# Kernel tuning notes

Hardware: AMD Instinct MI355X
Metric: run time of the kernel (lower is better)

## Reference

```python
import jax, jax.numpy as jnp
import numpy as np

B, S, D, H = 2, 2048, 2048, 16
DH = D // H  # 128
ROPE_BASE = 10000.0


def setup_inputs() -> dict:
    key = jax.random.key(0)
    ks = jax.random.split(key, 5)
    scale = 0.02
    return {
        "x": jax.random.normal(ks[0], (B, S, D), dtype=jnp.float32),
        "wq": jax.random.normal(ks[1], (D, D), dtype=jnp.float32) * scale,
        "wk": jax.random.normal(ks[2], (D, D), dtype=jnp.float32) * scale,
        "wv": jax.random.normal(ks[3], (D, D), dtype=jnp.float32) * scale,
        "wo": jax.random.normal(ks[4], (D, D), dtype=jnp.float32) * scale,
    }


def _rope_cache(seq_len, dhead):
    # flash-attn RotaryEmbedding: inv_freq over even dims, full rotary_dim = dhead
    inv_freq = 1.0 / (ROPE_BASE ** (jnp.arange(0, dhead, 2, dtype=jnp.float32) / dhead))
    t = jnp.arange(seq_len, dtype=jnp.float32)
    freqs = jnp.einsum("s,d->sd", t, inv_freq)  # [S, DH/2]
    return jnp.cos(freqs), jnp.sin(freqs)


def _apply_rope_interleaved(t, cos, sin):
    # t: [B, S, H, DH]; interleaved pairs (t[...,0::2], t[...,1::2])
    te, to = t[..., 0::2], t[..., 1::2]
    c = cos[None, :, None, :]
    s = sin[None, :, None, :]
    re = te * c - to * s
    ro = te * s + to * c
    return jnp.stack([re, ro], axis=-1).reshape(t.shape)


def reference(x, wq, wk, wv, wo):
    b, s, d = x.shape
    q = (x @ wq).reshape(b, s, H, DH)
    k = (x @ wk).reshape(b, s, H, DH)
    v = (x @ wv).reshape(b, s, H, DH)

    cos, sin = _rope_cache(s, DH)
    q = _apply_rope_interleaved(q.astype(jnp.float32), cos, sin)
    k = _apply_rope_interleaved(k.astype(jnp.float32), cos, sin)

    # flash_attn_func(causal=True) semantics: bf16 inputs, fp32 softmax, scale 1/sqrt(dhead)
    qb = q.astype(jnp.bfloat16)
    kb = k.astype(jnp.bfloat16)
    vb = v.astype(jnp.bfloat16)
    scale = 1.0 / np.sqrt(DH)
    scores = jnp.einsum("bqhd,bkhd->bhqk", qb, kb,
                        preferred_element_type=jnp.float32) * scale
    causal = jnp.tril(jnp.ones((s, s), dtype=bool))
    scores = jnp.where(causal[None, None], scores, -jnp.inf)
    p = jax.nn.softmax(scores, axis=-1)  # fp32
    attn = jnp.einsum("bhqk,bkhd->bqhd", p.astype(jnp.bfloat16), vb,
                      preferred_element_type=jnp.float32)
    attn = attn.astype(jnp.bfloat16).astype(x.dtype)  # flash returns bf16, then .to(x)
    out = attn.reshape(b, s, d) @ wo
    return out
```

## Files before the change

### kernel.cpp

```cpp
#include <hip/hip_runtime.h>
#include <hip/hip_bf16.h>
#include <stdint.h>

#define B_SZ   2
#define S_LEN  2048
#define DMODEL 2048
#define NH     16
#define DHD    128

typedef __attribute__((ext_vector_type(8))) __bf16 bf16x8;
typedef __attribute__((ext_vector_type(4))) float  f32x4;
typedef __attribute__((ext_vector_type(4))) float  float4v;
typedef __attribute__((ext_vector_type(8))) unsigned short ushort8;
typedef __attribute__((ext_vector_type(4))) unsigned short ushort4v;

__device__ __forceinline__ unsigned short f2bf(float f) {
  unsigned int u = __float_as_uint(f);
  unsigned int r = (u + 0x7fffu + ((u >> 16) & 1u)) >> 16;
  return (unsigned short)r;
}

__device__ __forceinline__ unsigned int cvt_pk_bf16(float lo, float hi) {
  unsigned int r;
  asm("v_cvt_pk_bf16_f32 %0, %1, %2" : "=v"(r) : "v"(lo), "v"(hi));
  return r;
}

__device__ __forceinline__ void async_cp16(void* lds, const void* g) {
  __builtin_amdgcn_global_load_lds(
      (const __attribute__((address_space(1))) void*)g,
      (__attribute__((address_space(3))) void*)lds, 16, 0, 0);
}

__global__ __launch_bounds__(256) void k_cast_bf16(const float* __restrict__ in,
                                                   unsigned short* __restrict__ out,
                                                   int n4) {
  int i = blockIdx.x * 256 + threadIdx.x;
  if (i >= n4) return;
  float4v v = ((const float4v*)in)[i];
  ushort4v o;
  o[0] = f2bf(v[0]); o[1] = f2bf(v[1]); o[2] = f2bf(v[2]); o[3] = f2bf(v[3]);
  ((ushort4v*)out)[i] = o;
}

__global__ __launch_bounds__(256) void k_transpose_all(const float* __restrict__ w0,
                                                       const float* __restrict__ w1,
                                                       const float* __restrict__ w2,
                                                       const float* __restrict__ w3,
                                                       unsigned short* __restrict__ WTbase) {
  __shared__ unsigned short tile[64 * 72];
  const int z = blockIdx.z;
  const float* W = (z == 0) ? w0 : (z == 1) ? w1 : (z == 2) ? w2 : w3;
  unsigned short* WT = WTbase + (size_t)z * 4194304;
  const int n0 = blockIdx.x * 64;
  const int k0 = blockIdx.y * 64;
  const int t = threadIdx.x;
#pragma unroll
  for (int i = 0; i < 4; ++i) {
    int c = t + 256 * i;
    int r = c >> 4, c4 = c & 15;
    float4v v = *(const float4v*)(W + (size_t)(k0 + r) * DMODEL + n0 + c4 * 4);
    ushort4v o;
    o[0] = f2bf(v[0]); o[1] = f2bf(v[1]); o[2] = f2bf(v[2]); o[3] = f2bf(v[3]);
    *(ushort4v*)(&tile[r * 72 + c4 * 4]) = o;
  }
  __syncthreads();
#pragma unroll
  for (int i = 0; i < 2; ++i) {
    int c = t + 256 * i;
    int n = c >> 3, k8 = c & 7;
    ushort8 o;
#pragma unroll
    for (int j = 0; j < 8; ++j) o[j] = tile[(k8 * 8 + j) * 72 + n];
    *(ushort8*)(WT + (size_t)(n0 + n) * DMODEL + k0 + k8 * 8) = o;
  }
}

__global__ __launch_bounds__(256) void k_rope_table(float* __restrict__ cosT,
                                                    float* __restrict__ sinT) {
  int i = blockIdx.x * 256 + threadIdx.x;
  int s = i >> 6, dj = i & 63;
  float e = __expf(-9.210340371976184f * (float)dj * (1.0f / 64.0f));
  float f = (float)s * e;
  cosT[i] = cosf(f);
  sinT[i] = sinf(f);
}

template <int EPI>
__global__ __launch_bounds__(512, 2) void k_gemm128(
    const unsigned short* __restrict__ A,
    const unsigned short* __restrict__ BT,
    float* __restrict__ C0,
    unsigned short* __restrict__ Cq,
    unsigned short* __restrict__ Ck,
    unsigned short* __restrict__ Cv,
    const float* __restrict__ cosT,
    const float* __restrict__ sinT,
    int chn) {
  __shared__ char smem[98304];
  const int tid = threadIdx.x;

  const int xcd = blockIdx.x & 7;
  const int idx = blockIdx.x >> 3;
  const int bm = (xcd >> 2) * 16 + (idx & 15);
  const int bn = (xcd & 3) * chn + (idx >> 4);

  const int gs = (tid & 7) ^ ((tid >> 3) & 7);
  const unsigned short* Abase = A + (size_t)(bm * 128 + (tid >> 3)) * 2048 + gs * 8;
  const unsigned short* Bbase = BT + (size_t)(bn * 256 + (tid >> 3)) * 2048 + gs * 8;
  const int dstA = tid * 16;
  const int dstB = 16384 + tid * 16;

  const int lane = tid & 63, wid = tid >> 6;
  const int wr = wid >> 2, wcn = wid & 3;
  const int lr = lane & 15, hi = lane >> 4;
  int aoff[4][2], boff[4][2];
#pragma unroll
  for (int m = 0; m < 4; ++m) {
    int row = wr * 64 + m * 16 + lr;
#pragma unroll
    for (int k = 0; k < 2; ++k)
      aoff[m][k] = row * 128 + ((((k * 4 + hi)) ^ (row & 7)) << 4);
  }
#pragma unroll
  for (int n = 0; n < 4; ++n) {
    int row = wcn * 64 + n * 16 + lr;
#pragma unroll
    for (int k = 0; k < 2; ++k)
      boff[n][k] = 16384 + row * 128 + ((((k * 4 + hi)) ^ (row & 7)) << 4);
  }

  f32x4 acc[4][4];
#pragma unroll
  for (int m = 0; m < 4; ++m)
#pragma unroll
    for (int n = 0; n < 4; ++n) {
      f32x4 z = {0.f, 0.f, 0.f, 0.f};
      acc[m][n] = z;
    }

#define STG_A(c, t_) do {                                                   \
    const unsigned short* _s = Abase + (t_) * 64;                           \
    async_cp16(smem + (c) * 49152 + dstA, _s);                              \
    async_cp16(smem + (c) * 49152 + dstA + 8192, _s + 64 * 2048);           \
  } while (0)
#define STG_B(c, t_) do {                                                   \
    const unsigned short* _s = Bbase + (t_) * 64;                           \
    async_cp16(smem + (c) * 49152 + dstB, _s);                              \
    async_cp16(smem + (c) * 49152 + dstB + 8192, _s + 64 * 2048);           \
    async_cp16(smem + (c) * 49152 + dstB + 16384, _s + 128 * 2048);         \
    async_cp16(smem + (c) * 49152 + dstB + 24576, _s + 192 * 2048);         \
  } while (0)

  auto tile = [&](int T, int CC, bool DO_A, bool DO_B, int VM) __attribute__((always_inline)) {
    const char* Sb = smem + CC * 49152;
    bf16x8 a0[4], b0[4], a1[4], b1[4];
#pragma unroll
    for (int m = 0; m < 4; ++m) a0[m] = *(const bf16x8*)(Sb + aoff[m][0]);
#pragma unroll
    for (int n = 0; n < 4; ++n) b0[n] = *(const bf16x8*)(Sb + boff[n][0]);
    if (DO_A) STG_A(CC ^ 1, T + 1);
    asm volatile("s_waitcnt lgkmcnt(0)" ::: "memory");
    __builtin_amdgcn_sched_barrier(0);
    __builtin_amdgcn_s_setprio(1);
#pragma unroll
    for (int m = 0; m < 4; ++m) {
      acc[m][0] = __builtin_amdgcn_mfma_f32_16x16x32_bf16(a0[m], b0[0], acc[m][0], 0, 0, 0);
      acc[m][1] = __builtin_amdgcn_mfma_f32_16x16x32_bf16(a0[m], b0[1], acc[m][1], 0, 0, 0);
    }
    __builtin_amdgcn_s_setprio(0);
    __builtin_amdgcn_sched_barrier(0);
#pragma unroll
    for (int m = 0; m < 4; ++m) a1[m] = *(const bf16x8*)(Sb + aoff[m][1]);
#pragma unroll
    for (int n = 0; n < 4; ++n) b1[n] = *(const bf16x8*)(Sb + boff[n][1]);
    __builtin_amdgcn_sched_barrier(0);
    __builtin_amdgcn_s_setprio(1);
#pragma unroll
    for (int m = 0; m < 4; ++m) {
      acc[m][2] = __builtin_amdgcn_mfma_f32_16x16x32_bf16(a0[m], b0[2], acc[m][2], 0, 0, 0);
      acc[m][3] = __builtin_amdgcn_mfma_f32_16x16x32_bf16(a0[m], b0[3], acc[m][3], 0, 0, 0);
    }
    __builtin_amdgcn_s_setprio(0);
    __builtin_amdgcn_s_barrier();
    __builtin_amdgcn_sched_barrier(0);
    asm volatile("s_waitcnt lgkmcnt(0)" ::: "memory");
    __builtin_amdgcn_sched_barrier(0);
    if (DO_B) STG_B(CC, T + 2);
    __builtin_amdgcn_s_setprio(1);
#pragma unroll
    for (int m = 0; m < 4; ++m)
#pragma unroll
      for (int n = 0; n < 4; ++n)
        acc[m][n] = __builtin_amdgcn_mfma_f32_16x16x32_bf16(a1[m], b1[n], acc[m][n], 0, 0, 0);
    __builtin_amdgcn_s_setprio(0);
    if (VM == 0) asm volatile("s_waitcnt vmcnt(4)" ::: "memory");
    else if (VM == 1) asm volatile("s_waitcnt vmcnt(0)" ::: "memory");
    if (VM != 2) {
      __builtin_amdgcn_s_barrier();
      __builtin_amdgcn_sched_barrier(0);
    }
  };

  STG_B(0, 0);
  STG_A(0, 0);
  STG_B(1, 1);
  asm volatile("s_waitcnt vmcnt(4)" ::: "memory");
  __builtin_amdgcn_s_barrier();
  __builtin_amdgcn_sched_barrier(0);

  for (int it = 0; it < 15; ++it) {
    tile(2 * it, 0, true, true, 0);
    tile(2 * it + 1, 1, true, true, 0);
  }
  tile(30, 0, true, false, 1);
  tile(31, 1, false, false, 2);

  const int row_b = bm * 128 + wr * 64 + hi * 4;
  const int col_b = bn * 256 + wcn * 64 + lr;
  if (EPI == 0) {
#pragma unroll
    for (int m = 0; m < 4; ++m)
#pragma unroll
      for (int n = 0; n < 4; ++n) {
        int col = col_b + n * 16;
#pragma unroll
        for (int j = 0; j < 4; ++j) {
          int row = row_b + m * 16 + j;
          C0[(size_t)row * 2048 + col] = acc[m][n][j];
        }
      }
  } else {
    const int sel = bn >> 3;
#pragma unroll
    for (int m = 0; m < 4; ++m) {
#pragma unroll
      for (int n = 0; n < 4; ++n) {
        int col = col_b + n * 16;
        int hh = (col >> 7) & 15, d = col & 127;
        if (sel == 2) {
#pragma unroll
          for (int j = 0; j < 4; ++j) {
            int row = row_b + m * 16 + j;
            int b = row >> 11, s = row & 2047;
            Cv[((size_t)(b * NH + hh) * S_LEN + s) * DHD + d] = f2bf(acc[m][n][j]);
          }
        } else {
          unsigned short* dst = sel ? Ck : Cq;
          int dj = d >> 1;
          float sgn = (d & 1) ? 1.f : -1.f;
#pragma unroll
          for (int j = 0; j < 4; ++j) {
            int row = row_b + m * 16 + j;
            int b = row >> 11, s = row & 2047;
            float v = acc[m][n][j];
            float pp = __shfl_xor(v, 1);
            float cc = cosT[(s << 6) + dj];
            float sn = sinT[(s << 6) + dj];
            dst[((size_t)(b * NH + hh) * S_LEN + s) * DHD + d] = f2bf(v * cc + sgn * pp * sn);
          }
        }
      }
    }
  }
#undef STG_A
#undef STG_B
}

__global__ __launch_bounds__(256) void k_flash_attn(const unsigned short* __restrict__ Qg,
                                                    const unsigned short* __restrict__ Kg,
                                                    const unsigned short* __restrict__ Vg,
                                                    unsigned short* __restrict__ Og) {
  __shared__ unsigned short K_lds[2][64 * 128];
  __shared__ unsigned short VT_lds[2][128 * 64];

  const int pq = blockIdx.x, h = blockIdx.y, b = blockIdx.z;
  const int t = threadIdx.x;
  const int lane = t & 63, wave = t >> 6;
  const int hi = lane >> 4, lr = lane & 15;

  const size_t head = (size_t)(b * NH + h) * (size_t)(S_LEN * DHD);
  const unsigned short* Q = Qg + head;
  const unsigned short* Kp = Kg + head;
  const unsigned short* Vp = Vg + head;

  const int kr0 = t >> 4;
  const int kgc = (t & 15) ^ (kr0 & 7);
  const unsigned short* Kbase = Kp + (size_t)kr0 * DHD + kgc * 8;
  const int kdst = t * 16;

  const int vdc = t & 15, vsp0 = t >> 4;
  const unsigned short* Vbase = Vp + (size_t)(2 * vsp0) * DHD + vdc * 8;
  const int bo0 = 16 * ((vsp0 >> 1) & 3) + 8 * ((vsp0 >> 3) & 1) + 4 * (vsp0 & 1);

  const float sc = 0.08838834764831845f;

  for (int pass = 0; pass < 2; ++pass) {
    const int qt = (pass == 0) ? pq : (15 - pq);
    const int nt = 2 * (qt + 1);
    const int qb0 = qt * 128 + wave * 16;
    const int qb1 = qb0 + 64;

    bf16x8 qf0[4], qf1[4];
    {
      const unsigned short* qr0 = Q + (size_t)(qb0 + lr) * DHD;
      const unsigned short* qr1 = Q + (size_t)(qb1 + lr) * DHD;
#pragma unroll
      for (int kc = 0; kc < 4; ++kc) {
        qf0[kc] = *(const bf16x8*)(qr0 + kc * 32 + hi * 8);
        qf1[kc] = *(const bf16x8*)(qr1 + kc * 32 + hi * 8);
      }
    }

    f32x4 of0[8], of1[8];
#pragma unroll
    for (int i = 0; i < 8; ++i) {
      f32x4 z = {0.f, 0.f, 0.f, 0.f};
      of0[i] = z;
      of1[i] = z;
    }
    float mS0 = -INFINITY, mS1 = -INFINITY;
    float ls0 = 0.f, ls1 = 0.f;

    {
#pragma unroll
      for (int i = 0; i < 4; ++i)
        async_cp16((char*)K_lds[0] + kdst + i * 4096, Kbase + (size_t)(16 * i) * DHD);
      ushort8 va0 = *(const ushort8*)(Vbase);
      ushort8 vb0 = *(const ushort8*)(Vbase + DHD);
      ushort8 va1 = *(const ushort8*)(Vbase + (size_t)32 * DHD);
      ushort8 vb1 = *(const ushort8*)(Vbase + (size_t)33 * DHD);
#pragma unroll
      for (int j = 0; j < 8; ++j) {
        int row = vdc * 8 + j;
        int swz = ((j ^ vdc) & 7) << 4;
        *(unsigned int*)((char*)VT_lds[0] + row * 128 + (bo0 ^ swz)) =
            (unsigned int)va0[j] | ((unsigned int)vb0[j] << 16);
        *(unsigned int*)((char*)VT_lds[0] + row * 128 + ((bo0 | 64) ^ swz)) =
            (unsigned int)va1[j] | ((unsigned int)vb1[j] << 16);
      }
    }
    __syncthreads();

    for (int tt = 0; tt < nt; ++tt) {
      const int cur = tt & 1;
      const int kv0 = tt * 64;
      const bool more = (tt + 1 < nt);

      ushort8 va0, vb0, va1, vb1;
      if (more) {
        const unsigned short* ks = Kbase + (size_t)(kv0 + 64) * DHD;
#pragma unroll
        for (int i = 0; i < 4; ++i)
          async_cp16((char*)K_lds[cur ^ 1] + kdst + i * 4096, ks + (size_t)(16 * i) * DHD);
        const unsigned short* vs = Vbase + (size_t)(kv0 + 64) * DHD;
        va0 = *(const ushort8*)(vs);
        vb0 = *(const ushort8*)(vs + DHD);
        va1 = *(const ushort8*)(vs + (size_t)32 * DHD);
        vb1 = *(const ushort8*)(vs + (size_t)33 * DHD);
      }

      const char* Kb = (const char*)K_lds[cur];
      f32x4 sf0[4], sf1[4];
#pragma unroll
      for (int n = 0; n < 4; ++n) {
        f32x4 z = {0.f, 0.f, 0.f, 0.f};
        sf0[n] = z;
        sf1[n] = z;
      }
      __builtin_amdgcn_s_setprio(1);
#pragma unroll
      for (int n = 0; n < 4; ++n) {
        const int kr = n * 16 + lr;
        const int kswz = (kr & 7) << 4;
#pragma unroll
        for (int kc = 0; kc < 4; ++kc) {
          bf16x8 kf = *(const bf16x8*)(Kb + kr * 256 + ((kc * 64 + hi * 16) ^ kswz));
          sf0[n] = __builtin_amdgcn_mfma_f32_16x16x32_bf16(kf, qf0[kc], sf0[n], 0, 0, 0);
          sf1[n] = __builtin_amdgcn_mfma_f32_16x16x32_bf16(kf, qf1[kc], sf1[n], 0, 0, 0);
        }
      }
      __builtin_amdgcn_s_setprio(0);

      unsigned int pk0[4][2], pk1[4][2];
      float cb0[4], cb1[4];
      const bool act0 = kv0 <= qb0 + 15;
      const bool act1 = kv0 <= qb1 + 15;

#define SOFTMAX_SET(SF, MS, LS, PK, CB, QB, ACT) do {                        \
    if (ACT) {                                                               \
      float p_[4][4];                                                        \
      float mx = -INFINITY;                                                  \
      const int qrow_ = (QB) + lr;                                           \
      if (kv0 + 63 > (QB)) {                                                 \
        _Pragma("unroll")                                                    \
        for (int n = 0; n < 4; ++n)                                          \
          _Pragma("unroll")                                                  \
          for (int j = 0; j < 4; ++j) {                                      \
            int kvcol = kv0 + n * 16 + hi * 4 + j;                           \
            float v = (kvcol > qrow_) ? -INFINITY : SF[n][j];                \
            p_[n][j] = v;                                                    \
            mx = fmaxf(mx, v);                                               \
          }                                                                  \
      } else {                                                               \
        _Pragma("unroll")                                                    \
        for (int n = 0; n < 4; ++n)                                          \
          _Pragma("unroll")                                                  \
          for (int j = 0; j < 4; ++j) {                                      \
            float v = SF[n][j];                                              \
            p_[n][j] = v;                                                    \
            mx = fmaxf(mx, v);                                               \
          }                                                                  \
      }                                                                      \
      mx = fmaxf(mx, __shfl_xor(mx, 16));                                    \
      mx = fmaxf(mx, __shfl_xor(mx, 32));                                    \
      float mn = fmaxf(MS, mx);                                              \
      float corr = __expf((MS - mn) * sc);                                   \
      MS = mn;                                                               \
      float mns = mn * sc;                                                   \
      float rs = 0.f;                                                        \
      _Pragma("unroll")                                                      \
      for (int n = 0; n < 4; ++n)                                            \
        _Pragma("unroll")                                                    \
        for (int j = 0; j < 4; ++j) {                                        \
          float e = __expf(__builtin_fmaf(p_[n][j], sc, -mns));              \
          p_[n][j] = e;                                                      \
          rs += e;                                                           \
        }                                                                    \
      rs += __shfl_xor(rs, 16);                                              \
      rs += __shfl_xor(rs, 32);                                              \
      LS = LS * corr + rs;                                                   \
      _Pragma("unroll")                                                      \
      for (int n = 0; n < 4; ++n) {                                          \
        PK[n][0] = cvt_pk_bf16(p_[n][0], p_[n][1]);                          \
        PK[n][1] = cvt_pk_bf16(p_[n][2], p_[n][3]);                          \
      }                                                                      \
      _Pragma("unroll")                                                      \
      for (int j = 0; j < 4; ++j) CB[j] = __shfl(corr, hi * 4 + j);          \
    } else {                                                                 \
      _Pragma("unroll")                                                      \
      for (int n = 0; n < 4; ++n) { PK[n][0] = 0u; PK[n][1] = 0u; }          \
      _Pragma("unroll")                                                      \
      for (int j = 0; j < 4; ++j) CB[j] = 1.f;                               \
    }                                                                        \
  } while (0)

      SOFTMAX_SET(sf0, mS0, ls0, pk0, cb0, qb0, act0);
      SOFTMAX_SET(sf1, mS1, ls1, pk1, cb1, qb1, act1);
#undef SOFTMAX_SET

#pragma unroll
      for (int nd = 0; nd < 8; ++nd)
#pragma unroll
        for (int j = 0; j < 4; ++j) {
          of0[nd][j] *= cb0[j];
          of1[nd][j] *= cb1[j];
        }

      const char* Vb = (const char*)VT_lds[cur];
      __builtin_amdgcn_s_setprio(1);
#pragma unroll
      for (int kc = 0; kc < 2; ++kc) {
        union { unsigned int u[4]; bf16x8 v; } pa0, pa1;
        pa0.u[0] = pk0[2 * kc][0];     pa0.u[1] = pk0[2 * kc][1];
        pa0.u[2] = pk0[2 * kc + 1][0]; pa0.u[3] = pk0[2 * kc + 1][1];
        pa1.u[0] = pk1[2 * kc][0];     pa1.u[1] = pk1[2 * kc][1];
        pa1.u[2] = pk1[2 * kc + 1][0]; pa1.u[3] = pk1[2 * kc + 1][1];
#pragma unroll
        for (int nd = 0; nd < 8; ++nd) {
          const int vr = nd * 16 + lr;
          const int vswz = ((vr & 7) ^ ((vr >> 3) & 7)) << 4;
          bf16x8 vf = *(const bf16x8*)(Vb + vr * 128 + ((kc * 64 + hi * 16) ^ vswz));
          of0[nd] = __builtin_amdgcn_mfma_f32_16x16x32_bf16(pa0.v, vf, of0[nd], 0, 0, 0);
          of1[nd] = __builtin_amdgcn_mfma_f32_16x16x32_bf16(pa1.v, vf, of1[nd], 0, 0, 0);
        }
      }
      __builtin_amdgcn_s_setprio(0);

      if (more) {
        char* Vw = (char*)VT_lds[cur ^ 1];
#pragma unroll
        for (int j = 0; j < 8; ++j) {
          int row = vdc * 8 + j;
          int swz = ((j ^ vdc) & 7) << 4;
          *(unsigned int*)(Vw + row * 128 + (bo0 ^ swz)) =
              (unsigned int)va0[j] | ((unsigned int)vb0[j] << 16);
          *(unsigned int*)(Vw + row * 128 + ((bo0 | 64) ^ swz)) =
              (unsigned int)va1[j] | ((unsigned int)vb1[j] << 16);
        }
      }
      __syncthreads();
    }

    float inv0[4], inv1[4];
#pragma unroll
    for (int j = 0; j < 4; ++j) {
      inv0[j] = 1.0f / __shfl(ls0, hi * 4 + j);
      inv1[j] = 1.0f / __shfl(ls1, hi * 4 + j);
    }
#pragma unroll
    for (int nd = 0; nd < 8; ++nd)
#pragma unroll
      for (int j = 0; j < 4; ++j) {
        int qr0 = qb0 + hi * 4 + j;
        int qr1 = qb1 + hi * 4 + j;
        Og[((size_t)(b * S_LEN + qr0) * NH + h) * DHD + nd * 16 + lr] = f2bf(of0[nd][j] * inv0[j]);
        Og[((size_t)(b * S_LEN + qr1) * NH + h) * DHD + nd * 16 + lr] = f2bf(of1[nd][j] * inv1[j]);
      }
  }
}

extern "C" void kernel_launch(void* const* d_in, const int* in_sizes, int n_in,
                              void* d_out, int out_size, void* d_ws, size_t ws_size,
                              hipStream_t stream) {
  const float* x  = (const float*)d_in[0];
  const float* wq = (const float*)d_in[1];
  const float* wk = (const float*)d_in[2];
  const float* wv = (const float*)d_in[3];
  const float* wo = (const float*)d_in[4];
  float* out = (float*)d_out;

  char* ws = (char*)d_ws;
  unsigned short* xb    = (unsigned short*)(ws);
  unsigned short* wqT   = (unsigned short*)(ws + 16777216);
  unsigned short* woT   = (unsigned short*)(ws + 41943040);
  unsigned short* qb    = (unsigned short*)(ws + 50331648);
  unsigned short* kb    = (unsigned short*)(ws + 67108864);
  unsigned short* vb    = (unsigned short*)(ws + 83886080);
  float*          cosT  = (float*)(ws + 100663296);
  float*          sinT  = (float*)(ws + 101187584);
  unsigned short* attnb = xb;

  k_cast_bf16<<<8192, 256, 0, stream>>>(x, xb, 2097152);
  dim3 tg(32, 32, 4);
  k_transpose_all<<<tg, 256, 0, stream>>>(wq, wk, wv, wo, wqT);
  k_rope_table<<<512, 256, 0, stream>>>(cosT, sinT);

  k_gemm128<1><<<768, 512, 0, stream>>>(xb, wqT, nullptr, qb, kb, vb, cosT, sinT, 6);

  dim3 ga(8, 16, 2);
  k_flash_attn<<<ga, 256, 0, stream>>>(qb, kb, vb, attnb);

  k_gemm128<0><<<256, 512, 0, stream>>>(attnb, woT, out, nullptr, nullptr, nullptr,
                                        nullptr, nullptr, 2);
}
```

Baseline: 258.1 us.

## Use 256x256 QKV GEMM tiles, flatten flash-attn grid, hoist LDS fragment loads

```diff
diff --git a/kernel.cpp b/kernel.cpp
--- a/kernel.cpp
+++ b/kernel.cpp
@@ -86,16 +86,161 @@
   sinT[i] = sinf(f);
 }
 
-template <int EPI>
+__global__ __launch_bounds__(512, 2) void k_gemm256(
+    const unsigned short* __restrict__ A,
+    const unsigned short* __restrict__ BT,
+    unsigned short* __restrict__ Cq,
+    unsigned short* __restrict__ Ck,
+    unsigned short* __restrict__ Cv,
+    const float* __restrict__ cosT,
+    const float* __restrict__ sinT) {
+  __shared__ char smem[131072];
+  const int tid = threadIdx.x;
+
+  const int xcd = blockIdx.x & 7;
+  const int idx = blockIdx.x >> 3;
+  const int bm = (xcd >> 1) * 4 + (idx & 3);
+  const int bn = (xcd & 1) * 12 + (idx >> 2);
+
+  const int gs = (tid & 7) ^ ((tid >> 3) & 7);
+  const unsigned short* Abase = A + (size_t)(bm * 256 + (tid >> 3)) * 2048 + gs * 8;
+  const unsigned short* Bbase = BT + (size_t)(bn * 256 + (tid >> 3)) * 2048 + gs * 8;
+  const int dstA = tid * 16;
+  const int dstB = 32768 + tid * 16;
+
+  const int lane = tid & 63, wid = tid >> 6;
+  const int wr = wid >> 2, wcn = wid & 3;
+  const int lr = lane & 15, hi = lane >> 4;
+  const int sw0 = ((hi) ^ (lr & 7)) << 4;
+  const int sw1 = ((4 + hi) ^ (lr & 7)) << 4;
+  const int aB0 = (wr * 128 + lr) * 128 + sw0;
+  const int aB1 = (wr * 128 + lr) * 128 + sw1;
+  const int bB0 = 32768 + (wcn * 64 + lr) * 128 + sw0;
+  const int bB1 = 32768 + (wcn * 64 + lr) * 128 + sw1;
+
+  f32x4 acc[8][4];
+#pragma unroll
+  for (int m = 0; m < 8; ++m)
+#pragma unroll
+    for (int n = 0; n < 4; ++n) {
+      f32x4 z = {0.f, 0.f, 0.f, 0.f};
+      acc[m][n] = z;
+    }
+
+#define STG_A6(c, t_) do {                                                  \
+    const unsigned short* _s = Abase + (t_) * 64;                           \
+    async_cp16(smem + (c) * 65536 + dstA, _s);                              \
+    async_cp16(smem + (c) * 65536 + dstA + 8192, _s + (size_t)64 * 2048);   \
+    async_cp16(smem + (c) * 65536 + dstA + 16384, _s + (size_t)128 * 2048); \
+    async_cp16(smem + (c) * 65536 + dstA + 24576, _s + (size_t)192 * 2048); \
+  } while (0)
+#define STG_B6(c, t_) do {                                                  \
+    const unsigned short* _s = Bbase + (t_) * 64;                           \
+    async_cp16(smem + (c) * 65536 + dstB, _s);                              \
+    async_cp16(smem + (c) * 65536 + dstB + 8192, _s + (size_t)64 * 2048);   \
+    async_cp16(smem + (c) * 65536 + dstB + 16384, _s + (size_t)128 * 2048); \
+    async_cp16(smem + (c) * 65536 + dstB + 24576, _s + (size_t)192 * 2048); \
+  } while (0)
+
+  auto tile = [&](int T, int CC, bool DO_A, bool DO_B, int VM) __attribute__((always_inline)) {
+    const char* Sb = smem + CC * 65536;
+    bf16x8 a0[8], b0[4], b1[4];
+#pragma unroll
+    for (int n = 0; n < 4; ++n) b0[n] = *(const bf16x8*)(Sb + bB0 + n * 2048);
+#pragma unroll
+    for (int m = 0; m < 8; ++m) a0[m] = *(const bf16x8*)(Sb + aB0 + m * 2048);
+#pragma unroll
+    for (int n = 0; n < 4; ++n) b1[n] = *(const bf16x8*)(Sb + bB1 + n * 2048);
+    if (DO_A) STG_A6(CC ^ 1, T + 1);
+    asm volatile("s_waitcnt lgkmcnt(4)" ::: "memory");
+    __builtin_amdgcn_sched_barrier(0);
+    __builtin_amdgcn_s_setprio(1);
+#pragma unroll
+    for (int m = 0; m < 8; ++m)
+#pragma unroll
+      for (int n = 0; n < 4; ++n)
+        acc[m][n] = __builtin_amdgcn_mfma_f32_16x16x32_bf16(a0[m], b0[n], acc[m][n], 0, 0, 0);
+    __builtin_amdgcn_s_setprio(0);
+    __builtin_amdgcn_s_barrier();
+    __builtin_amdgcn_sched_barrier(0);
+    asm volatile("s_waitcnt lgkmcnt(0)" ::: "memory");
+    __builtin_amdgcn_sched_barrier(0);
+    if (DO_B) STG_B6(CC, T + 2);
+    bf16x8 a1[8];
+#pragma unroll
+    for (int m = 0; m < 8; ++m) a1[m] = *(const bf16x8*)(Sb + aB1 + m * 2048);
+    asm volatile("s_waitcnt lgkmcnt(0)" ::: "memory");
+    __builtin_amdgcn_sched_barrier(0);
+    __builtin_amdgcn_s_setprio(1);
+#pragma unroll
+    for (int m = 0; m < 8; ++m)
+#pragma unroll
+      for (int n = 0; n < 4; ++n)
+        acc[m][n] = __builtin_amdgcn_mfma_f32_16x16x32_bf16(a1[m], b1[n], acc[m][n], 0, 0, 0);
+    __builtin_amdgcn_s_setprio(0);
+    if (VM == 0) asm volatile("s_waitcnt vmcnt(4)" ::: "memory");
+    else if (VM == 1) asm volatile("s_waitcnt vmcnt(0)" ::: "memory");
+    if (VM != 2) {
+      __builtin_amdgcn_s_barrier();
+      __builtin_amdgcn_sched_barrier(0);
+    }
+  };
+
+  STG_B6(0, 0);
+  STG_A6(0, 0);
+  STG_B6(1, 1);
+  asm volatile("s_waitcnt vmcnt(4)" ::: "memory");
+  __builtin_amdgcn_s_barrier();
+  __builtin_amdgcn_sched_barrier(0);
+
+  for (int it = 0; it < 15; ++it) {
+    tile(2 * it, 0, true, true, 0);
+    tile(2 * it + 1, 1, true, true, 0);
+  }
+  tile(30, 0, true, false, 1);
+  tile(31, 1, false, false, 2);
+
+  const int row_b = bm * 256 + wr * 128 + hi * 4;
+  const int col_b = bn * 256 + wcn * 64 + lr;
+  const int sel = bn >> 3;
+#pragma unroll
+  for (int m = 0; m < 8; ++m) {
+#pragma unroll
+    for (int n = 0; n < 4; ++n) {
+      int col = col_b + n * 16;
+      int hh = (col >> 7) & 15, d = col & 127;
+      if (sel == 2) {
+#pragma unroll
+        for (int j = 0; j < 4; ++j) {
+          int row = row_b + m * 16 + j;
+          int b = row >> 11, s = row & 2047;
+          Cv[((size_t)(b * NH + hh) * S_LEN + s) * DHD + d] = f2bf(acc[m][n][j]);
+        }
+      } else {
+        unsigned short* dst = sel ? Ck : Cq;
+        int dj = d >> 1;
+        float sgn = (d & 1) ? 1.f : -1.f;
+#pragma unroll
+        for (int j = 0; j < 4; ++j) {
+          int row = row_b + m * 16 + j;
+          int b = row >> 11, s = row & 2047;
+          float v = acc[m][n][j];
+          float pp = __shfl_xor(v, 1);
+          float cc = cosT[(s << 6) + dj];
+          float sn = sinT[(s << 6) + dj];
+          dst[((size_t)(b * NH + hh) * S_LEN + s) * DHD + d] = f2bf(v * cc + sgn * pp * sn);
+        }
+      }
+    }
+  }
+#undef STG_A6
+#undef STG_B6
+}
+
 __global__ __launch_bounds__(512, 2) void k_gemm128(
     const unsigned short* __restrict__ A,
     const unsigned short* __restrict__ BT,
     float* __restrict__ C0,
-    unsigned short* __restrict__ Cq,
-    unsigned short* __restrict__ Ck,
-    unsigned short* __restrict__ Cv,
-    const float* __restrict__ cosT,
-    const float* __restrict__ sinT,
     int chn) {
   __shared__ char smem[98304];
   const int tid = threadIdx.x;
@@ -159,28 +304,20 @@
     for (int m = 0; m < 4; ++m) a0[m] = *(const bf16x8*)(Sb + aoff[m][0]);
 #pragma unroll
     for (int n = 0; n < 4; ++n) b0[n] = *(const bf16x8*)(Sb + boff[n][0]);
+    __builtin_amdgcn_sched_barrier(0);
+#pragma unroll
+    for (int m = 0; m < 4; ++m) a1[m] = *(const bf16x8*)(Sb + aoff[m][1]);
+#pragma unroll
+    for (int n = 0; n < 4; ++n) b1[n] = *(const bf16x8*)(Sb + boff[n][1]);
     if (DO_A) STG_A(CC ^ 1, T + 1);
-    asm volatile("s_waitcnt lgkmcnt(0)" ::: "memory");
+    asm volatile("s_waitcnt lgkmcnt(8)" ::: "memory");
     __builtin_amdgcn_sched_barrier(0);
     __builtin_amdgcn_s_setprio(1);
 #pragma unroll
-    for (int m = 0; m < 4; ++m) {
-      acc[m][0] = __builtin_amdgcn_mfma_f32_16x16x32_bf16(a0[m], b0[0], acc[m][0], 0, 0, 0);
-      acc[m][1] = __builtin_amdgcn_mfma_f32_16x16x32_bf16(a0[m], b0[1], acc[m][1], 0, 0, 0);
-    }
-    __builtin_amdgcn_s_setprio(0);
-    __builtin_amdgcn_sched_barrier(0);
-#pragma unroll
-    for (int m = 0; m < 4; ++m) a1[m] = *(const bf16x8*)(Sb + aoff[m][1]);
-#pragma unroll
-    for (int n = 0; n < 4; ++n) b1[n] = *(const bf16x8*)(Sb + boff[n][1]);
-    __builtin_amdgcn_sched_barrier(0);
-    __builtin_amdgcn_s_setprio(1);
-#pragma unroll
-    for (int m = 0; m < 4; ++m) {
-      acc[m][2] = __builtin_amdgcn_mfma_f32_16x16x32_bf16(a0[m], b0[2], acc[m][2], 0, 0, 0);
-      acc[m][3] = __builtin_amdgcn_mfma_f32_16x16x32_bf16(a0[m], b0[3], acc[m][3], 0, 0, 0);
-    }
+    for (int m = 0; m < 4; ++m)
+#pragma unroll
+      for (int n = 0; n < 4; ++n)
+        acc[m][n] = __builtin_amdgcn_mfma_f32_16x16x32_bf16(a0[m], b0[n], acc[m][n], 0, 0, 0);
     __builtin_amdgcn_s_setprio(0);
     __builtin_amdgcn_s_barrier();
     __builtin_amdgcn_sched_barrier(0);
@@ -218,51 +355,17 @@
 
   const int row_b = bm * 128 + wr * 64 + hi * 4;
   const int col_b = bn * 256 + wcn * 64 + lr;
-  if (EPI == 0) {
-#pragma unroll
-    for (int m = 0; m < 4; ++m)
-#pragma unroll
-      for (int n = 0; n < 4; ++n) {
-        int col = col_b + n * 16;
-#pragma unroll
-        for (int j = 0; j < 4; ++j) {
-          int row = row_b + m * 16 + j;
-          C0[(size_t)row * 2048 + col] = acc[m][n][j];
-        }
+#pragma unroll
+  for (int m = 0; m < 4; ++m)
+#pragma unroll
+    for (int n = 0; n < 4; ++n) {
+      int col = col_b + n * 16;
+#pragma unroll
+      for (int j = 0; j < 4; ++j) {
+        int row = row_b + m * 16 + j;
+        C0[(size_t)row * 2048 + col] = acc[m][n][j];
       }
-  } else {
-    const int sel = bn >> 3;
-#pragma unroll
-    for (int m = 0; m < 4; ++m) {
-#pragma unroll
-      for (int n = 0; n < 4; ++n) {
-        int col = col_b + n * 16;
-        int hh = (col >> 7) & 15, d = col & 127;
-        if (sel == 2) {
-#pragma unroll
-          for (int j = 0; j < 4; ++j) {
-            int row = row_b + m * 16 + j;
-            int b = row >> 11, s = row & 2047;
-            Cv[((size_t)(b * NH + hh) * S_LEN + s) * DHD + d] = f2bf(acc[m][n][j]);
-          }
-        } else {
-          unsigned short* dst = sel ? Ck : Cq;
-          int dj = d >> 1;
-          float sgn = (d & 1) ? 1.f : -1.f;
-#pragma unroll
-          for (int j = 0; j < 4; ++j) {
-            int row = row_b + m * 16 + j;
-            int b = row >> 11, s = row & 2047;
-            float v = acc[m][n][j];
-            float pp = __shfl_xor(v, 1);
-            float cc = cosT[(s << 6) + dj];
-            float sn = sinT[(s << 6) + dj];
-            dst[((size_t)(b * NH + hh) * S_LEN + s) * DHD + d] = f2bf(v * cc + sgn * pp * sn);
-          }
-        }
-      }
-    }
-  }
+    }
 #undef STG_A
 #undef STG_B
 }
@@ -274,7 +377,14 @@
   __shared__ unsigned short K_lds[2][64 * 128];
   __shared__ unsigned short VT_lds[2][128 * 64];
 
-  const int pq = blockIdx.x, h = blockIdx.y, b = blockIdx.z;
+  const int bx = blockIdx.x;
+  const int half = bx >> 8;
+  const int j5 = bx & 255;
+  const int ti = j5 >> 5;
+  const int hb = j5 & 31;
+  const int h = hb & 15, b = hb >> 4;
+  const int qt = half ? ti : (15 - ti);
+
   const int t = threadIdx.x;
   const int lane = t & 63, wave = t >> 6;
   const int hi = lane >> 4, lr = lane & 15;
@@ -295,97 +405,95 @@
 
   const float sc = 0.08838834764831845f;
 
-  for (int pass = 0; pass < 2; ++pass) {
-    const int qt = (pass == 0) ? pq : (15 - pq);
-    const int nt = 2 * (qt + 1);
-    const int qb0 = qt * 128 + wave * 16;
-    const int qb1 = qb0 + 64;
-
-    bf16x8 qf0[4], qf1[4];
-    {
-      const unsigned short* qr0 = Q + (size_t)(qb0 + lr) * DHD;
-      const unsigned short* qr1 = Q + (size_t)(qb1 + lr) * DHD;
+  const int nt = 2 * (qt + 1);
+  const int qb0 = qt * 128 + wave * 16;
+  const int qb1 = qb0 + 64;
+
+  bf16x8 qf0[4], qf1[4];
+  {
+    const unsigned short* qr0 = Q + (size_t)(qb0 + lr) * DHD;
+    const unsigned short* qr1 = Q + (size_t)(qb1 + lr) * DHD;
+#pragma unroll
+    for (int kc = 0; kc < 4; ++kc) {
+      qf0[kc] = *(const bf16x8*)(qr0 + kc * 32 + hi * 8);
+      qf1[kc] = *(const bf16x8*)(qr1 + kc * 32 + hi * 8);
+    }
+  }
+
+  f32x4 of0[8], of1[8];
+#pragma unroll
+  for (int i = 0; i < 8; ++i) {
+    f32x4 z = {0.f, 0.f, 0.f, 0.f};
+    of0[i] = z;
+    of1[i] = z;
+  }
+  float mS0 = -INFINITY, mS1 = -INFINITY;
+  float ls0 = 0.f, ls1 = 0.f;
+
+  {
+#pragma unroll
+    for (int i = 0; i < 4; ++i)
+      async_cp16((char*)K_lds[0] + kdst + i * 4096, Kbase + (size_t)(16 * i) * DHD);
+    ushort8 va0 = *(const ushort8*)(Vbase);
+    ushort8 vb0 = *(const ushort8*)(Vbase + DHD);
+    ushort8 va1 = *(const ushort8*)(Vbase + (size_t)32 * DHD);
+    ushort8 vb1 = *(const ushort8*)(Vbase + (size_t)33 * DHD);
+#pragma unroll
+    for (int j = 0; j < 8; ++j) {
+      int row = vdc * 8 + j;
+      int swz = ((j ^ vdc) & 7) << 4;
+      *(unsigned int*)((char*)VT_lds[0] + row * 128 + (bo0 ^ swz)) =
+          (unsigned int)va0[j] | ((unsigned int)vb0[j] << 16);
+      *(unsigned int*)((char*)VT_lds[0] + row * 128 + ((bo0 | 64) ^ swz)) =
+          (unsigned int)va1[j] | ((unsigned int)vb1[j] << 16);
+    }
+  }
+  __syncthreads();
+
+  for (int tt = 0; tt < nt; ++tt) {
+    const int cur = tt & 1;
+    const int kv0 = tt * 64;
+    const bool more = (tt + 1 < nt);
+
+    ushort8 va0, vb0, va1, vb1;
+    if (more) {
+      const unsigned short* ks = Kbase + (size_t)(kv0 + 64) * DHD;
+#pragma unroll
+      for (int i = 0; i < 4; ++i)
+        async_cp16((char*)K_lds[cur ^ 1] + kdst + i * 4096, ks + (size_t)(16 * i) * DHD);
+      const unsigned short* vs = Vbase + (size_t)(kv0 + 64) * DHD;
+      va0 = *(const ushort8*)(vs);
+      vb0 = *(const ushort8*)(vs + DHD);
+      va1 = *(const ushort8*)(vs + (size_t)32 * DHD);
+      vb1 = *(const ushort8*)(vs + (size_t)33 * DHD);
+    }
+
+    const char* Kb = (const char*)K_lds[cur];
+    f32x4 sf0[4], sf1[4];
+#pragma unroll
+    for (int n = 0; n < 4; ++n) {
+      f32x4 z = {0.f, 0.f, 0.f, 0.f};
+      sf0[n] = z;
+      sf1[n] = z;
+    }
+    __builtin_amdgcn_s_setprio(1);
+#pragma unroll
+    for (int n = 0; n < 4; ++n) {
+      const int kr = n * 16 + lr;
+      const int kswz = (kr & 7) << 4;
 #pragma unroll
       for (int kc = 0; kc < 4; ++kc) {
-        qf0[kc] = *(const bf16x8*)(qr0 + kc * 32 + hi * 8);
-        qf1[kc] = *(const bf16x8*)(qr1 + kc * 32 + hi * 8);
+        bf16x8 kf = *(const bf16x8*)(Kb + kr * 256 + ((kc * 64 + hi * 16) ^ kswz));
+        sf0[n] = __builtin_amdgcn_mfma_f32_16x16x32_bf16(kf, qf0[kc], sf0[n], 0, 0, 0);
+        sf1[n] = __builtin_amdgcn_mfma_f32_16x16x32_bf16(kf, qf1[kc], sf1[n], 0, 0, 0);
       }
     }
-
-    f32x4 of0[8], of1[8];
-#pragma unroll
-    for (int i = 0; i < 8; ++i) {
-      f32x4 z = {0.f, 0.f, 0.f, 0.f};
-      of0[i] = z;
-      of1[i] = z;
-    }
-    float mS0 = -INFINITY, mS1 = -INFINITY;
-    float ls0 = 0.f, ls1 = 0.f;
-
-    {
-#pragma unroll
-      for (int i = 0; i < 4; ++i)
-        async_cp16((char*)K_lds[0] + kdst + i * 4096, Kbase + (size_t)(16 * i) * DHD);
-      ushort8 va0 = *(const ushort8*)(Vbase);
-      ushort8 vb0 = *(const ushort8*)(Vbase + DHD);
-      ushort8 va1 = *(const ushort8*)(Vbase + (size_t)32 * DHD);
-      ushort8 vb1 = *(const ushort8*)(Vbase + (size_t)33 * DHD);
-#pragma unroll
-      for (int j = 0; j < 8; ++j) {
-        int row = vdc * 8 + j;
-        int swz = ((j ^ vdc) & 7) << 4;
-        *(unsigned int*)((char*)VT_lds[0] + row * 128 + (bo0 ^ swz)) =
-            (unsigned int)va0[j] | ((unsigned int)vb0[j] << 16);
-        *(unsigned int*)((char*)VT_lds[0] + row * 128 + ((bo0 | 64) ^ swz)) =
-            (unsigned int)va1[j] | ((unsigned int)vb1[j] << 16);
-      }
-    }
-    __syncthreads();
-
-    for (int tt = 0; tt < nt; ++tt) {
-      const int cur = tt & 1;
-      const int kv0 = tt * 64;
-      const bool more = (tt + 1 < nt);
-
-      ushort8 va0, vb0, va1, vb1;
-      if (more) {
-        const unsigned short* ks = Kbase + (size_t)(kv0 + 64) * DHD;
-#pragma unroll
-        for (int i = 0; i < 4; ++i)
-          async_cp16((char*)K_lds[cur ^ 1] + kdst + i * 4096, ks + (size_t)(16 * i) * DHD);
-        const unsigned short* vs = Vbase + (size_t)(kv0 + 64) * DHD;
-        va0 = *(const ushort8*)(vs);
-        vb0 = *(const ushort8*)(vs + DHD);
-        va1 = *(const ushort8*)(vs + (size_t)32 * DHD);
-        vb1 = *(const ushort8*)(vs + (size_t)33 * DHD);
-      }
-
-      const char* Kb = (const char*)K_lds[cur];
-      f32x4 sf0[4], sf1[4];
-#pragma unroll
-      for (int n = 0; n < 4; ++n) {
-        f32x4 z = {0.f, 0.f, 0.f, 0.f};
-        sf0[n] = z;
-        sf1[n] = z;
-      }
-      __builtin_amdgcn_s_setprio(1);
-#pragma unroll
-      for (int n = 0; n < 4; ++n) {
-        const int kr = n * 16 + lr;
-        const int kswz = (kr & 7) << 4;
-#pragma unroll
-        for (int kc = 0; kc < 4; ++kc) {
-          bf16x8 kf = *(const bf16x8*)(Kb + kr * 256 + ((kc * 64 + hi * 16) ^ kswz));
-          sf0[n] = __builtin_amdgcn_mfma_f32_16x16x32_bf16(kf, qf0[kc], sf0[n], 0, 0, 0);
-          sf1[n] = __builtin_amdgcn_mfma_f32_16x16x32_bf16(kf, qf1[kc], sf1[n], 0, 0, 0);
-        }
-      }
-      __builtin_amdgcn_s_setprio(0);
-
-      unsigned int pk0[4][2], pk1[4][2];
-      float cb0[4], cb1[4];
-      const bool act0 = kv0 <= qb0 + 15;
-      const bool act1 = kv0 <= qb1 + 15;
+    __builtin_amdgcn_s_setprio(0);
+
+    unsigned int pk0[4][2], pk1[4][2];
+    float cb0[4], cb1[4];
+    const bool act0 = kv0 <= qb0 + 15;
+    const bool act1 = kv0 <= qb1 + 15;
 
 #define SOFTMAX_SET(SF, MS, LS, PK, CB, QB, ACT) do {                        \
     if (ACT) {                                                               \
@@ -445,69 +553,68 @@
     }                                                                        \
   } while (0)
 
-      SOFTMAX_SET(sf0, mS0, ls0, pk0, cb0, qb0, act0);
-      SOFTMAX_SET(sf1, mS1, ls1, pk1, cb1, qb1, act1);
+    SOFTMAX_SET(sf0, mS0, ls0, pk0, cb0, qb0, act0);
+    SOFTMAX_SET(sf1, mS1, ls1, pk1, cb1, qb1, act1);
 #undef SOFTMAX_SET
 
 #pragma unroll
-      for (int nd = 0; nd < 8; ++nd)
-#pragma unroll
-        for (int j = 0; j < 4; ++j) {
-          of0[nd][j] *= cb0[j];
-          of1[nd][j] *= cb1[j];
-        }
-
-      const char* Vb = (const char*)VT_lds[cur];
-      __builtin_amdgcn_s_setprio(1);
-#pragma unroll
-      for (int kc = 0; kc < 2; ++kc) {
-        union { unsigned int u[4]; bf16x8 v; } pa0, pa1;
-        pa0.u[0] = pk0[2 * kc][0];     pa0.u[1] = pk0[2 * kc][1];
-        pa0.u[2] = pk0[2 * kc + 1][0]; pa0.u[3] = pk0[2 * kc + 1][1];
-        pa1.u[0] = pk1[2 * kc][0];     pa1.u[1] = pk1[2 * kc][1];
-        pa1.u[2] = pk1[2 * kc + 1][0]; pa1.u[3] = pk1[2 * kc + 1][1];
-#pragma unroll
-        for (int nd = 0; nd < 8; ++nd) {
-          const int vr = nd * 16 + lr;
-          const int vswz = ((vr & 7) ^ ((vr >> 3) & 7)) << 4;
-          bf16x8 vf = *(const bf16x8*)(Vb + vr * 128 + ((kc * 64 + hi * 16) ^ vswz));
-          of0[nd] = __builtin_amdgcn_mfma_f32_16x16x32_bf16(pa0.v, vf, of0[nd], 0, 0, 0);
-          of1[nd] = __builtin_amdgcn_mfma_f32_16x16x32_bf16(pa1.v, vf, of1[nd], 0, 0, 0);
-        }
+    for (int nd = 0; nd < 8; ++nd)
+#pragma unroll
+      for (int j = 0; j < 4; ++j) {
+        of0[nd][j] *= cb0[j];
+        of1[nd][j] *= cb1[j];
       }
-      __builtin_amdgcn_s_setprio(0);
-
-      if (more) {
-        char* Vw = (char*)VT_lds[cur ^ 1];
-#pragma unroll
-        for (int j = 0; j < 8; ++j) {
-          int row = vdc * 8 + j;
-          int swz = ((j ^ vdc) & 7) << 4;
-          *(unsigned int*)(Vw + row * 128 + (bo0 ^ swz)) =
-              (unsigned int)va0[j] | ((unsigned int)vb0[j] << 16);
-          *(unsigned int*)(Vw + row * 128 + ((bo0 | 64) ^ swz)) =
-              (unsigned int)va1[j] | ((unsigned int)vb1[j] << 16);
-        }
+
+    const char* Vb = (const char*)VT_lds[cur];
+    __builtin_amdgcn_s_setprio(1);
+#pragma unroll
+    for (int kc = 0; kc < 2; ++kc) {
+      union { unsigned int u[4]; bf16x8 v; } pa0, pa1;
+      pa0.u[0] = pk0[2 * kc][0];     pa0.u[1] = pk0[2 * kc][1];
+      pa0.u[2] = pk0[2 * kc + 1][0]; pa0.u[3] = pk0[2 * kc + 1][1];
+      pa1.u[0] = pk1[2 * kc][0];     pa1.u[1] = pk1[2 * kc][1];
+      pa1.u[2] = pk1[2 * kc + 1][0]; pa1.u[3] = pk1[2 * kc + 1][1];
+#pragma unroll
+      for (int nd = 0; nd < 8; ++nd) {
+        const int vr = nd * 16 + lr;
+        const int vswz = ((vr & 7) ^ ((vr >> 3) & 7)) << 4;
+        bf16x8 vf = *(const bf16x8*)(Vb + vr * 128 + ((kc * 64 + hi * 16) ^ vswz));
+        of0[nd] = __builtin_amdgcn_mfma_f32_16x16x32_bf16(pa0.v, vf, of0[nd], 0, 0, 0);
+        of1[nd] = __builtin_amdgcn_mfma_f32_16x16x32_bf16(pa1.v, vf, of1[nd], 0, 0, 0);
       }
-      __syncthreads();
-    }
-
-    float inv0[4], inv1[4];
+    }
+    __builtin_amdgcn_s_setprio(0);
+
+    if (more) {
+      char* Vw = (char*)VT_lds[cur ^ 1];
+#pragma unroll
+      for (int j = 0; j < 8; ++j) {
+        int row = vdc * 8 + j;
+        int swz = ((j ^ vdc) & 7) << 4;
+        *(unsigned int*)(Vw + row * 128 + (bo0 ^ swz)) =
+            (unsigned int)va0[j] | ((unsigned int)vb0[j] << 16);
+        *(unsigned int*)(Vw + row * 128 + ((bo0 | 64) ^ swz)) =
+            (unsigned int)va1[j] | ((unsigned int)vb1[j] << 16);
+      }
+    }
+    __syncthreads();
+  }
+
+  float inv0[4], inv1[4];
+#pragma unroll
+  for (int j = 0; j < 4; ++j) {
+    inv0[j] = 1.0f / __shfl(ls0, hi * 4 + j);
+    inv1[j] = 1.0f / __shfl(ls1, hi * 4 + j);
+  }
+#pragma unroll
+  for (int nd = 0; nd < 8; ++nd)
 #pragma unroll
     for (int j = 0; j < 4; ++j) {
-      inv0[j] = 1.0f / __shfl(ls0, hi * 4 + j);
-      inv1[j] = 1.0f / __shfl(ls1, hi * 4 + j);
-    }
-#pragma unroll
-    for (int nd = 0; nd < 8; ++nd)
-#pragma unroll
-      for (int j = 0; j < 4; ++j) {
-        int qr0 = qb0 + hi * 4 + j;
-        int qr1 = qb1 + hi * 4 + j;
-        Og[((size_t)(b * S_LEN + qr0) * NH + h) * DHD + nd * 16 + lr] = f2bf(of0[nd][j] * inv0[j]);
-        Og[((size_t)(b * S_LEN + qr1) * NH + h) * DHD + nd * 16 + lr] = f2bf(of1[nd][j] * inv1[j]);
-      }
-  }
+      int qr0 = qb0 + hi * 4 + j;
+      int qr1 = qb1 + hi * 4 + j;
+      Og[((size_t)(b * S_LEN + qr0) * NH + h) * DHD + nd * 16 + lr] = f2bf(of0[nd][j] * inv0[j]);
+      Og[((size_t)(b * S_LEN + qr1) * NH + h) * DHD + nd * 16 + lr] = f2bf(of1[nd][j] * inv1[j]);
+    }
 }
 
 extern "C" void kernel_launch(void* const* d_in, const int* in_sizes, int n_in,
@@ -536,11 +643,9 @@
   k_transpose_all<<<tg, 256, 0, stream>>>(wq, wk, wv, wo, wqT);
   k_rope_table<<<512, 256, 0, stream>>>(cosT, sinT);
 
-  k_gemm128<1><<<768, 512, 0, stream>>>(xb, wqT, nullptr, qb, kb, vb, cosT, sinT, 6);
-
-  dim3 ga(8, 16, 2);
-  k_flash_attn<<<ga, 256, 0, stream>>>(qb, kb, vb, attnb);
-
-  k_gemm128<0><<<256, 512, 0, stream>>>(attnb, woT, out, nullptr, nullptr, nullptr,
-                                        nullptr, nullptr, 2);
-}
+  k_gemm256<<<384, 512, 0, stream>>>(xb, wqT, qb, kb, vb, cosT, sinT);
+
+  k_flash_attn<<<512, 256, 0, stream>>>(qb, kb, vb, attnb);
+
+  k_gemm128<<<256, 512, 0, stream>>>(attnb, woT, out, 2);
+}
```

New measurement: 287.1 us. 11.2% more time.
